# Kernel tuning notes

Hardware: AMD Instinct MI355X
Metric: run time of the kernel (lower is better)

Reference implementation:

```python
import jax, jax.numpy as jnp
import numpy as np

NUM_NODES, WINDOW, DIM, B = 50000, 8, 256, 8192


def setup_inputs() -> dict:
    key = jax.random.key(0)
    k1, k2, k3, k4, k5, k6 = jax.random.split(key, 6)
    return {
        "bank": jax.random.normal(k1, (NUM_NODES, WINDOW, DIM), dtype=jnp.float32),
        "timestamps": jax.random.uniform(k2, (NUM_NODES, WINDOW), dtype=jnp.float32),
        "neighbor_repr": jax.random.normal(k3, (B, DIM), dtype=jnp.float32),
        "t": jax.random.uniform(k4, (B,), dtype=jnp.float32) * 1000.0,
        "ptr": jax.random.randint(k5, (NUM_NODES,), 0, 1000000, dtype=jnp.int64) if jax.config.jax_enable_x64 else jax.random.randint(k5, (NUM_NODES,), 0, 1000000, dtype=jnp.int32),
        "idx": jax.random.randint(k6, (B,), 0, NUM_NODES, dtype=jnp.int32),
    }


def reference(bank, timestamps, neighbor_repr, t, ptr, idx):
    """Vectorized equivalent of NeighborhoodEvolutionBank.write().

    The torch loop writes batch elements sequentially: the k-th occurrence of a
    node index within the batch lands in slot (ptr[node] + k) % window, and ptr
    is bumped once per occurrence. We reproduce that by computing, for each
    batch element, its rank among earlier duplicates of the same index.
    """
    window = bank.shape[1]
    # rank[bi] = number of j < bi with idx[j] == idx[bi]  (B x B, B=8192 -> 64M bool, fine)
    eq = idx[:, None] == idx[None, :]
    rank = jnp.sum(jnp.tril(eq, k=-1), axis=1).astype(ptr.dtype)  # [B]
    slot = (ptr[idx] + rank) % window                              # [B]

    bank_new = bank.at[idx, slot].set(neighbor_repr)               # fused scatter write
    ts_new = timestamps.at[idx, slot].set(t.astype(timestamps.dtype))
    ptr_new = ptr.at[idx].add(1)
    return bank_new, ts_new, ptr_new
```

## Files before the change

### kernel.cpp

```cpp
#include <hip/hip_runtime.h>

#define NUM_NODES 50000
#define WINDOW 8
#define DIM 256
#define BATCH 8192

__global__ void count_kernel(const int* __restrict__ idx, int* __restrict__ count) {
    int bi = blockIdx.x * blockDim.x + threadIdx.x;
    if (bi < BATCH) atomicAdd(&count[idx[bi]], 1);
}

__global__ void rank_kernel(const int* __restrict__ idx, const int* __restrict__ ptr,
                            const int* __restrict__ count, int* __restrict__ slotcode) {
    __shared__ int sidx[BATCH];
    __shared__ int anyneed;
    int tid = threadIdx.x;
    int bi  = blockIdx.x * blockDim.x + tid;

    int node = idx[bi];
    int c    = count[node];
    bool need = (c > 1);

    if (tid == 0) anyneed = 0;
    __syncthreads();
    if (need) anyneed = 1;
    __syncthreads();

    if (anyneed) {
        for (int j = tid; j < BATCH; j += blockDim.x) sidx[j] = idx[j];
        __syncthreads();
    }

    int rank = 0;
    if (need) {
        for (int j = 0; j < bi; ++j) rank += (sidx[j] == node);
    }

    int slot = (ptr[node] + rank) & (WINDOW - 1);
    int win  = (rank >= c - WINDOW);
    slotcode[bi] = win ? (node * WINDOW + slot) : -1;
}

__global__ void scatter_kernel(const int* __restrict__ slotcode,
                               const float* __restrict__ nrep,
                               const float* __restrict__ t,
                               float* __restrict__ out_bank,
                               float* __restrict__ out_ts) {
    int bi   = blockIdx.x;
    int code = slotcode[bi];
    if (code < 0) return;
    int lane = threadIdx.x;
    const float4* src = (const float4*)(nrep + (size_t)bi * DIM);
    float4*       dst = (float4*)(out_bank + (size_t)code * DIM);
    dst[lane] = src[lane];
    if (lane == 0) out_ts[code] = t[bi];
}

__global__ void ptr_kernel(const int* __restrict__ ptr, const int* __restrict__ count,
                           float* __restrict__ out_ptr) {
    int n = blockIdx.x * blockDim.x + threadIdx.x;
    if (n < NUM_NODES) out_ptr[n] = (float)(ptr[n] + count[n]);
}

extern "C" void kernel_launch(void* const* d_in, const int* in_sizes, int n_in,
                              void* d_out, int out_size, void* d_ws, size_t ws_size,
                              hipStream_t stream) {
    const float* bank       = (const float*)d_in[0];
    const float* timestamps = (const float*)d_in[1];
    const float* nrep       = (const float*)d_in[2];
    const float* t          = (const float*)d_in[3];
    const int*   ptr        = (const int*)  d_in[4];
    const int*   idx        = (const int*)  d_in[5];

    float* out_bank = (float*)d_out;
    float* out_ts   = out_bank + (size_t)NUM_NODES * WINDOW * DIM;
    float* out_ptr  = out_ts   + (size_t)NUM_NODES * WINDOW;

    int* count    = (int*)d_ws;
    int* slotcode = count + NUM_NODES;

    hipMemsetAsync(count, 0, NUM_NODES * sizeof(int), stream);

    count_kernel<<<(BATCH + 255) / 256, 256, 0, stream>>>(idx, count);
    rank_kernel<<<BATCH / 256, 256, 0, stream>>>(idx, ptr, count, slotcode);

    hipMemcpyAsync(out_bank, bank,
                   (size_t)NUM_NODES * WINDOW * DIM * sizeof(float),
                   hipMemcpyDeviceToDevice, stream);
    hipMemcpyAsync(out_ts, timestamps,
                   (size_t)NUM_NODES * WINDOW * sizeof(float),
                   hipMemcpyDeviceToDevice, stream);

    scatter_kernel<<<BATCH, 64, 0, stream>>>(slotcode, nrep, t, out_bank, out_ts);
    ptr_kernel<<<(NUM_NODES + 255) / 256, 256, 0, stream>>>(ptr, count, out_ptr);
}
```

Measured before the change: 263.8 us.

## Fuse bank copy and scatter into one winner-map gather kernel

Replaces the device-to-device memcpys plus the separate scatter kernel with a single grid-stride kernel. It copies each bank row, or substitutes the winning batch row, using a per-slot winner map filled by the rank kernel. This is meant to avoid writing the overwritten rows twice and to save two extra launches. In exchange it adds a memset of the winner map and a winner lookup per float4, and the copy now runs through a custom kernel instead of the runtime memcpy path.

Result: faster. 241.9 us (-8.3%).

```diff
diff --git a/kernel.cpp b/kernel.cpp
--- a/kernel.cpp
+++ b/kernel.cpp
@@ -11,7 +11,7 @@
 }
 
 __global__ void rank_kernel(const int* __restrict__ idx, const int* __restrict__ ptr,
-                            const int* __restrict__ count, int* __restrict__ slotcode) {
+                            const int* __restrict__ count, int* __restrict__ winner) {
     __shared__ int sidx[BATCH];
     __shared__ int anyneed;
     int tid = threadIdx.x;
@@ -36,24 +36,30 @@
         for (int j = 0; j < bi; ++j) rank += (sidx[j] == node);
     }
 
-    int slot = (ptr[node] + rank) & (WINDOW - 1);
-    int win  = (rank >= c - WINDOW);
-    slotcode[bi] = win ? (node * WINDOW + slot) : -1;
+    if (rank >= c - WINDOW) {
+        int slot = (ptr[node] + rank) & (WINDOW - 1);
+        winner[node * WINDOW + slot] = bi;
+    }
 }
 
-__global__ void scatter_kernel(const int* __restrict__ slotcode,
-                               const float* __restrict__ nrep,
-                               const float* __restrict__ t,
-                               float* __restrict__ out_bank,
-                               float* __restrict__ out_ts) {
-    int bi   = blockIdx.x;
-    int code = slotcode[bi];
-    if (code < 0) return;
-    int lane = threadIdx.x;
-    const float4* src = (const float4*)(nrep + (size_t)bi * DIM);
-    float4*       dst = (float4*)(out_bank + (size_t)code * DIM);
-    dst[lane] = src[lane];
-    if (lane == 0) out_ts[code] = t[bi];
+__global__ void __launch_bounds__(256)
+fused_copy_kernel(const float4* __restrict__ bank4,
+                  const float*  __restrict__ timestamps,
+                  const float4* __restrict__ nrep4,
+                  const float*  __restrict__ t,
+                  const int*    __restrict__ winner,
+                  float4* __restrict__ out_bank4,
+                  float*  __restrict__ out_ts) {
+    const long total = (long)NUM_NODES * WINDOW * (DIM / 4);
+    const long nth   = (long)gridDim.x * blockDim.x;
+    for (long i = (long)blockIdx.x * blockDim.x + threadIdx.x; i < total; i += nth) {
+        int  row = (int)(i >> 6);
+        int  w   = winner[row];
+        float4 v = (w >= 0) ? nrep4[(long)w * (DIM / 4) + (i & 63)] : bank4[i];
+        out_bank4[i] = v;
+        if ((i & 63) == 0)
+            out_ts[row] = (w >= 0) ? t[w] : timestamps[row];
+    }
 }
 
 __global__ void ptr_kernel(const int* __restrict__ ptr, const int* __restrict__ count,
@@ -76,21 +82,18 @@
     float* out_ts   = out_bank + (size_t)NUM_NODES * WINDOW * DIM;
     float* out_ptr  = out_ts   + (size_t)NUM_NODES * WINDOW;
 
-    int* count    = (int*)d_ws;
-    int* slotcode = count + NUM_NODES;
+    int* count  = (int*)d_ws;
+    int* winner = count + NUM_NODES;
 
     hipMemsetAsync(count, 0, NUM_NODES * sizeof(int), stream);
+    hipMemsetAsync(winner, 0xFF, (size_t)NUM_NODES * WINDOW * sizeof(int), stream);
 
     count_kernel<<<(BATCH + 255) / 256, 256, 0, stream>>>(idx, count);
-    rank_kernel<<<BATCH / 256, 256, 0, stream>>>(idx, ptr, count, slotcode);
+    rank_kernel<<<BATCH / 256, 256, 0, stream>>>(idx, ptr, count, winner);
 
-    hipMemcpyAsync(out_bank, bank,
-                   (size_t)NUM_NODES * WINDOW * DIM * sizeof(float),
-                   hipMemcpyDeviceToDevice, stream);
-    hipMemcpyAsync(out_ts, timestamps,
-                   (size_t)NUM_NODES * WINDOW * sizeof(float),
-                   hipMemcpyDeviceToDevice, stream);
+    fused_copy_kernel<<<2048, 256, 0, stream>>>(
+        (const float4*)bank, timestamps, (const float4*)nrep, t, winner,
+        (float4*)out_bank, out_ts);
 
-    scatter_kernel<<<BATCH, 64, 0, stream>>>(slotcode, nrep, t, out_bank, out_ts);
     ptr_kernel<<<(NUM_NODES + 255) / 256, 256, 0, stream>>>(ptr, count, out_ptr);
 }
```

## Rank only duplicate indices via compacted list; fuse bank copy with ptr update

Applied to the files above, without the earlier changes.

Replaces the per-block O(B) rank scan with a classify pass that assigns slots directly to unique indices and appends only duplicated batch positions to a compacted list. A single-block kernel then ranks those duplicates against each other. The hipMemcpy device-to-device copies and the ptr kernel are replaced by one grid-stride float4 copy kernel that also writes the updated ptr. The single-block duplicate ranking is quadratic in the number of duplicates, which is large for random indices over 50k nodes, and the hand-written copy may not match the copy engine's bandwidth.

New measurement: 844.5 us. +220.1%, slower.

```diff
diff --git a/kernel.cpp b/kernel.cpp
--- a/kernel.cpp
+++ b/kernel.cpp
@@ -4,62 +4,75 @@
 #define WINDOW 8
 #define DIM 256
 #define BATCH 8192
+#define BANK4 ((long)NUM_NODES * WINDOW * (DIM / 4))
+#define TS4   ((long)NUM_NODES * WINDOW / 4)
 
 __global__ void count_kernel(const int* __restrict__ idx, int* __restrict__ count) {
     int bi = blockIdx.x * blockDim.x + threadIdx.x;
     if (bi < BATCH) atomicAdd(&count[idx[bi]], 1);
 }
 
-__global__ void rank_kernel(const int* __restrict__ idx, const int* __restrict__ ptr,
-                            const int* __restrict__ count, int* __restrict__ slotcode) {
-    __shared__ int sidx[BATCH];
-    __shared__ int anyneed;
-    int tid = threadIdx.x;
-    int bi  = blockIdx.x * blockDim.x + tid;
-
+__global__ void classify_kernel(const int* __restrict__ idx, const int* __restrict__ ptr,
+                                const int* __restrict__ count,
+                                int* __restrict__ slotcode,
+                                int* __restrict__ duplist, int* __restrict__ dupN) {
+    int bi = blockIdx.x * blockDim.x + threadIdx.x;
+    if (bi >= BATCH) return;
     int node = idx[bi];
     int c    = count[node];
-    bool need = (c > 1);
+    if (c == 1) {
+        slotcode[bi] = node * WINDOW + (ptr[node] & (WINDOW - 1));
+    } else {
+        duplist[atomicAdd(dupN, 1)] = bi;
+    }
+}
 
-    if (tid == 0) anyneed = 0;
+__global__ void dup_rank_kernel(const int* __restrict__ idx, const int* __restrict__ ptr,
+                                const int* __restrict__ count,
+                                const int* __restrict__ duplist, const int* __restrict__ dupN,
+                                int* __restrict__ slotcode) {
+    __shared__ int spos[BATCH];
+    int n = *dupN;
+    for (int k = threadIdx.x; k < n; k += blockDim.x) spos[k] = duplist[k];
     __syncthreads();
-    if (need) anyneed = 1;
-    __syncthreads();
+    for (int k = threadIdx.x; k < n; k += blockDim.x) {
+        int p    = spos[k];
+        int node = idx[p];
+        int rank = 0;
+        for (int m = 0; m < n; ++m) {
+            int q = spos[m];
+            rank += (q < p && idx[q] == node);
+        }
+        int c = count[node];
+        slotcode[p] = (rank >= c - WINDOW)
+                      ? node * WINDOW + ((ptr[node] + rank) & (WINDOW - 1))
+                      : -1;
+    }
+}
 
-    if (anyneed) {
-        for (int j = tid; j < BATCH; j += blockDim.x) sidx[j] = idx[j];
-        __syncthreads();
-    }
-
-    int rank = 0;
-    if (need) {
-        for (int j = 0; j < bi; ++j) rank += (sidx[j] == node);
-    }
-
-    int slot = (ptr[node] + rank) & (WINDOW - 1);
-    int win  = (rank >= c - WINDOW);
-    slotcode[bi] = win ? (node * WINDOW + slot) : -1;
+__global__ void __launch_bounds__(256)
+copy_kernel(const float4* __restrict__ bank4, const float4* __restrict__ ts4,
+            const int* __restrict__ ptr, const int* __restrict__ count,
+            float4* __restrict__ out_bank4, float4* __restrict__ out_ts4,
+            float* __restrict__ out_ptr) {
+    const long tid = (long)blockIdx.x * blockDim.x + threadIdx.x;
+    const long nth = (long)gridDim.x * blockDim.x;
+    for (long i = tid; i < BANK4; i += nth) out_bank4[i] = bank4[i];
+    for (long i = tid; i < TS4;   i += nth) out_ts4[i]   = ts4[i];
+    if (tid < NUM_NODES) out_ptr[tid] = (float)(ptr[tid] + count[tid]);
 }
 
 __global__ void scatter_kernel(const int* __restrict__ slotcode,
-                               const float* __restrict__ nrep,
+                               const float4* __restrict__ nrep4,
                                const float* __restrict__ t,
-                               float* __restrict__ out_bank,
+                               float4* __restrict__ out_bank4,
                                float* __restrict__ out_ts) {
     int bi   = blockIdx.x;
     int code = slotcode[bi];
     if (code < 0) return;
     int lane = threadIdx.x;
-    const float4* src = (const float4*)(nrep + (size_t)bi * DIM);
-    float4*       dst = (float4*)(out_bank + (size_t)code * DIM);
-    dst[lane] = src[lane];
+    out_bank4[(size_t)code * (DIM / 4) + lane] = nrep4[(size_t)bi * (DIM / 4) + lane];
     if (lane == 0) out_ts[code] = t[bi];
-}
-
-__global__ void ptr_kernel(const int* __restrict__ ptr, const int* __restrict__ count,
-                           float* __restrict__ out_ptr) {
-    int n = blockIdx.x * blockDim.x + threadIdx.x;
-    if (n < NUM_NODES) out_ptr[n] = (float)(ptr[n] + count[n]);
 }
 
 extern "C" void kernel_launch(void* const* d_in, const int* in_sizes, int n_in,
@@ -77,20 +90,21 @@
     float* out_ptr  = out_ts   + (size_t)NUM_NODES * WINDOW;
 
     int* count    = (int*)d_ws;
-    int* slotcode = count + NUM_NODES;
+    int* dupN     = count + NUM_NODES;
+    int* duplist  = dupN + 1;
+    int* slotcode = duplist + BATCH;
 
-    hipMemsetAsync(count, 0, NUM_NODES * sizeof(int), stream);
+    hipMemsetAsync(count, 0, (NUM_NODES + 1) * sizeof(int), stream);
 
-    count_kernel<<<(BATCH + 255) / 256, 256, 0, stream>>>(idx, count);
-    rank_kernel<<<BATCH / 256, 256, 0, stream>>>(idx, ptr, count, slotcode);
+    count_kernel   <<<(BATCH + 255) / 256, 256, 0, stream>>>(idx, count);
+    classify_kernel<<<(BATCH + 255) / 256, 256, 0, stream>>>(idx, ptr, count,
+                                                             slotcode, duplist, dupN);
+    dup_rank_kernel<<<1, 256, 0, stream>>>(idx, ptr, count, duplist, dupN, slotcode);
 
-    hipMemcpyAsync(out_bank, bank,
-                   (size_t)NUM_NODES * WINDOW * DIM * sizeof(float),
-                   hipMemcpyDeviceToDevice, stream);
-    hipMemcpyAsync(out_ts, timestamps,
-                   (size_t)NUM_NODES * WINDOW * sizeof(float),
-                   hipMemcpyDeviceToDevice, stream);
+    copy_kernel<<<2048, 256, 0, stream>>>(
+        (const float4*)bank, (const float4*)timestamps, ptr, count,
+        (float4*)out_bank, (float4*)out_ts, out_ptr);
 
-    scatter_kernel<<<BATCH, 64, 0, stream>>>(slotcode, nrep, t, out_bank, out_ts);
-    ptr_kernel<<<(NUM_NODES + 255) / 256, 256, 0, stream>>>(ptr, count, out_ptr);
+    scatter_kernel<<<BATCH, 64, 0, stream>>>(slotcode, (const float4*)nrep, t,
+                                             (float4*)out_bank, out_ts);
 }
```
